# Performance work log

Hardware: AMD Instinct MI355X
Metric: run time of the kernel (lower is better)

The kernel has to match this reference:

```python
import jax, jax.numpy as jnp
import numpy as np


def _mlp(x, W1, b1, W2, b2):
    # x: (B, M, T); torch MLPLayer: transpose(1,2) -> Linear -> Linear -> LeakyReLU -> transpose back
    h = jnp.einsum('bmt,hm->bht', x, W1) + b1[None, :, None]   # (B, H, T)
    y = jnp.einsum('bht,oh->bot', h, W2) + b2[None, :, None]   # (B, M, T)
    return jax.nn.leaky_relu(y, negative_slope=0.01)


def _calc_attn(q, k, v):
    # q: (B, M, Tq), k: (B, M, Tk), v: (B, M, Tk)
    Tq = q.shape[-1]
    qk = jnp.einsum('bmq,bmk->bqk', q, k)                       # (B, Tq, Tk)
    eye = jnp.eye(Tq, dtype=qk.dtype)                           # broadcasts: (Tq,Tq) or (1,1)
    logits = jnp.exp(qk - qk * eye / jnp.sqrt(jnp.asarray(Tq, qk.dtype)))
    scores = jax.nn.softmax(logits, axis=-1)
    return jnp.einsum('bqk,bmk->bmq', scores, v)                # (B, M, Tq)


def setup_inputs() -> dict:
    key = jax.random.key(0)
    B, M, T, H = 16, 128, 2048, 512
    ks = jax.random.split(key, 14)
    s = 0.02
    inp = {
        'pattern': jax.random.normal(ks[0], (B, M, T), jnp.float32),
        'value': jax.random.normal(ks[1], (B, M, T), jnp.float32),
        'kernel_size': 33,
    }
    names = ['q', 'k', 'o']
    for i, n in enumerate(names):
        inp['W%s1' % n] = jax.random.normal(ks[2 + 4 * i], (H, M), jnp.float32) * s
        inp['b%s1' % n] = jax.random.normal(ks[3 + 4 * i], (H,), jnp.float32) * s
        inp['W%s2' % n] = jax.random.normal(ks[4 + 4 * i], (M, H), jnp.float32) * s
        inp['b%s2' % n] = jax.random.normal(ks[5 + 4 * i], (M,), jnp.float32) * s
    return inp


def reference(pattern, value, kernel_size, Wq1, bq1, Wq2, bq2, Wk1, bk1, Wk2, bk2, Wo1, bo1, Wo2, bo2):
    query = _mlp(pattern, Wq1, bq1, Wq2, bq2)
    key = _mlp(pattern, Wk1, bk1, Wk2, bk2)
    # full (internal) attention
    attn_in = _calc_attn(query, key, value)                     # (B, M, T)
    rep_in = _mlp(attn_in, Wo1, bo1, Wo2, bo2)
    # windowed (external) attention
    T = query.shape[-1]
    cu = (kernel_size - 1) // 2
    q_w = query[..., T - 1 - cu : T - cu]                       # (B, M, 1)
    k_w = key[..., kernel_size - cu - 1 : T - cu - 2]           # (B, M, T-k-1)
    v_w = value[..., kernel_size : T - 1]                       # (B, M, T-k-1)
    attn_ex = _calc_attn(q_w, k_w, v_w)                         # (B, M, 1)
    rep_ex = _mlp(attn_ex, Wo1, bo1, Wo2, bo2)
    return jnp.concatenate([rep_in, rep_ex], axis=-1)           # (B, M, T+1)
```

## Files before the change

### kernel.cpp

```cpp
#include <hip/hip_runtime.h>
#include <hip/hip_bf16.h>
#include <math.h>

#define B_    16
#define M_    128
#define T_    2048
#define H_    512
#define TOUT_ 2049

typedef unsigned short u16;
typedef unsigned int   u32;
typedef __bf16 bf16x8 __attribute__((ext_vector_type(8)));
typedef float  f32x16 __attribute__((ext_vector_type(16)));
typedef float  f32x4  __attribute__((ext_vector_type(4)));
typedef u32    u32x4  __attribute__((ext_vector_type(4)));
typedef u32    u32x2  __attribute__((ext_vector_type(2)));

#define A_OFF     0
#define C_OFF     16384
#define MEAN_OFF  16896
#define AQKBF_OFF 19200
#define AOBF_OFF  35584
#define QT_OFF    43776
#define KT_OFF    (43776 + 2097152)
#define VB_OFF    (43776 + 2 * 2097152)

static __device__ __forceinline__ u16 f2bf(float f) {
  u32 u = __float_as_uint(f);
  u = (u + 0x7FFFu + ((u >> 16) & 1u)) >> 16;
  return (u16)u;
}
static __device__ __forceinline__ u32 pk2(float lo, float hi) {
  __hip_bfloat162 h = __float22bfloat162_rn(float2{lo, hi});
  u32 r;
  __builtin_memcpy(&r, &h, 4);
  return r;
}
static __device__ __forceinline__ bf16x8 ldfrag(const u16* p) {
  return __builtin_bit_cast(bf16x8, *(const u32x4*)p);
}
static __device__ __forceinline__ float ex2(float x) {
#if __has_builtin(__builtin_amdgcn_exp2f)
  return __builtin_amdgcn_exp2f(x);
#else
  return exp2f(x);
#endif
}

__global__ __launch_bounds__(128) void fuse_weights_all(
    const float* __restrict__ W1q, const float* __restrict__ b1q,
    const float* __restrict__ W2q, const float* __restrict__ b2q,
    const float* __restrict__ W1k, const float* __restrict__ b1k,
    const float* __restrict__ W2k, const float* __restrict__ b2k,
    const float* __restrict__ W1o, const float* __restrict__ b1o,
    const float* __restrict__ W2o, const float* __restrict__ b2o,
    float* __restrict__ A, float* __restrict__ c,
    u16* __restrict__ Aqk_bf, u16* __restrict__ Ao_bf) {
  __shared__ float w2row[H_];
  int which = blockIdx.x >> 7;
  int o = blockIdx.x & 127;
  const float* W1 = which == 0 ? W1q : which == 1 ? W1k : W1o;
  const float* b1 = which == 0 ? b1q : which == 1 ? b1k : b1o;
  const float* W2 = which == 0 ? W2q : which == 1 ? W2k : W2o;
  const float* b2 = which == 0 ? b2q : which == 1 ? b2k : b2o;
  int m = threadIdx.x;
  for (int h = m; h < H_; h += 128) w2row[h] = W2[o * H_ + h];
  __syncthreads();
  float acc = 0.f;
#pragma unroll 8
  for (int h = 0; h < H_; ++h) acc = fmaf(w2row[h], W1[h * M_ + m], acc);
  u16 ab = f2bf(acc);
  if (which == 0)      Aqk_bf[o * 128 + m] = ab;
  else if (which == 1) Aqk_bf[(128 + o) * 128 + m] = ab;
  else               { Ao_bf[o * 128 + m] = ab; A[o * M_ + m] = acc; }
  if (m < 64) {
    float cc = 0.f;
    for (int h = m; h < H_; h += 64) cc = fmaf(w2row[h], b1[h], cc);
#pragma unroll
    for (int off = 32; off > 0; off >>= 1) cc += __shfl_down(cc, off, 64);
    if (m == 0) c[which * 128 + o] = cc + b2[o];
  }
}

#define XS 68

__global__ __launch_bounds__(256) void prep_kernel(
    const float* __restrict__ pattern, const u16* __restrict__ Aqk_bf,
    const float* __restrict__ cqk, u16* __restrict__ qT, u16* __restrict__ kT,
    const float* __restrict__ value, u16* __restrict__ vb,
    float* __restrict__ meanv) {
  __shared__ alignas(16) float xsf[128 * XS];
  int bx = blockIdx.x;
  int tid = threadIdx.x;

  if (bx >= 512) {
    int bm = bx - 512;
    float* red = xsf;
    const float* row = value + (size_t)bm * T_;
    int i0 = tid * 8;
    float4 a = *(const float4*)(row + i0);
    float4 bq = *(const float4*)(row + i0 + 4);
    u32x4 o = {pk2(a.x, a.y), pk2(a.z, a.w), pk2(bq.x, bq.y), pk2(bq.z, bq.w)};
    *(u32x4*)&vb[(size_t)bm * T_ + i0] = o;
    float vals[8] = {a.x, a.y, a.z, a.w, bq.x, bq.y, bq.z, bq.w};
    float s = 0.f;
#pragma unroll
    for (int j = 0; j < 8; ++j) {
      int idx = i0 + j;
      if (idx >= 33 && idx < T_ - 1) s += vals[j];
    }
    red[tid] = s;
    __syncthreads();
    for (int st = 128; st > 0; st >>= 1) {
      if (tid < st) red[tid] += red[tid + st];
      __syncthreads();
    }
    if (tid == 0) meanv[bm] = red[0] * (1.f / 2014.f);
    return;
  }

  int b = bx >> 5;
  int t0 = (bx & 31) * 64;
  int lane = tid & 63;
  int wv = tid >> 6;
  int l31 = lane & 31;
  int lh8 = (lane >> 5) * 8;

  bf16x8 afr[2][8];
#pragma unroll
  for (int i = 0; i < 2; ++i) {
    const u16* ap = Aqk_bf + ((2 * wv + i) * 32 + l31) * 128 + lh8;
#pragma unroll
    for (int s = 0; s < 8; ++s) afr[i][s] = ldfrag(ap + 16 * s);
  }

#pragma unroll
  for (int rep = 0; rep < 8; ++rep) {
    int m = rep * 16 + (tid >> 4);
    int tc = (tid & 15) * 4;
    float4 v = *(const float4*)&pattern[(size_t)(b * M_ + m) * T_ + t0 + tc];
    *(float4*)&xsf[m * XS + tc] = v;
  }
  __syncthreads();

  bf16x8 bfr[2][8];
#pragma unroll
  for (int tt = 0; tt < 2; ++tt) {
#pragma unroll
    for (int s = 0; s < 8; ++s) {
      float v0 = xsf[(s * 16 + lh8 + 0) * XS + tt * 32 + l31];
      float v1 = xsf[(s * 16 + lh8 + 1) * XS + tt * 32 + l31];
      float v2 = xsf[(s * 16 + lh8 + 2) * XS + tt * 32 + l31];
      float v3 = xsf[(s * 16 + lh8 + 3) * XS + tt * 32 + l31];
      float v4 = xsf[(s * 16 + lh8 + 4) * XS + tt * 32 + l31];
      float v5 = xsf[(s * 16 + lh8 + 5) * XS + tt * 32 + l31];
      float v6 = xsf[(s * 16 + lh8 + 6) * XS + tt * 32 + l31];
      float v7 = xsf[(s * 16 + lh8 + 7) * XS + tt * 32 + l31];
      u32x4 p = {pk2(v0, v1), pk2(v2, v3), pk2(v4, v5), pk2(v6, v7)};
      bfr[tt][s] = __builtin_bit_cast(bf16x8, p);
    }
  }
  __syncthreads();

  u16* obuf = (u16*)xsf;
#pragma unroll
  for (int tt = 0; tt < 2; ++tt) {
#pragma unroll
    for (int i = 0; i < 2; ++i) {
      f32x16 acc;
#pragma unroll
      for (int r = 0; r < 16; ++r) acc[r] = 0.f;
#pragma unroll
      for (int s = 0; s < 8; ++s)
        acc = __builtin_amdgcn_mfma_f32_32x32x16_bf16(afr[i][s], bfr[tt][s], acc, 0, 0, 0);
      int ot = 2 * wv + i;
      int t = tt * 32 + l31;
      float sc = (ot < 4) ? 1.44269504f : 1.0f;
#pragma unroll
      for (int r = 0; r < 16; ++r) {
        int orow = (r & 3) + 8 * (r >> 2) + 4 * (lane >> 5);
        float v = acc[r] + cqk[ot * 32 + orow];
        v = v > 0.f ? v : 0.01f * v;
        obuf[t * 258 + ot * 32 + orow] = f2bf(v * sc);
      }
    }
  }
  __syncthreads();

  const u32* ob32 = (const u32*)obuf;
#pragma unroll
  for (int g = 0; g < 8; ++g) {
    int G = wv * 8 + g;
    int mat = G >> 4;
    int t = (G & 15) * 4 + (lane >> 4);
    int og2 = lane & 15;
    int wbase = t * 129 + mat * 64 + og2 * 4;
    u32x4 vv = {ob32[wbase], ob32[wbase + 1], ob32[wbase + 2], ob32[wbase + 3]};
    u32* dst = (u32*)((mat ? kT : qT) + ((size_t)(b * T_ + t0 + t)) * 128) + og2 * 4;
    *(u32x4*)dst = vv;
  }
}

#define QSTR 136
#define VSTR 72
#define PSTR 72
#define PTSTR 136
#define KTILE 64
#define NKT  (T_ / KTILE)
#define CINIT 0.52876637f

__global__ __launch_bounds__(1024, 4) void attn_mfma_kernel(
    const u16* __restrict__ qT, const u16* __restrict__ kT,
    const u16* __restrict__ vB, const u16* __restrict__ Ao_bf,
    const float* __restrict__ co, const float* __restrict__ Aofp,
    const float* __restrict__ meanv, float* __restrict__ out) {
  extern __shared__ u16 smem[];
  u16* ks0 = smem;
  u16* ks1 = smem + 8704;
  u16* vs0 = smem + 17408;
  u16* vs1 = smem + 26624;
  u16* pls = smem + 35840;
  float* dls   = (float*)smem;
  u16*   ptbuf = smem + 17408;

  int b = blockIdx.y;
  int q0 = blockIdx.x * 128;
  int tid = threadIdx.x;
  int lane = tid & 63;
  int wv = tid >> 6;
  int l31 = lane & 31;
  int h = lane >> 5;
  int lh8 = h * 8;
  int qt = wv & 3;
  int ksl = wv >> 2;
  int mt = wv >> 2;

  const u16* gkb = kT + (size_t)b * T_ * 128;
  const u16* gvb = vB + (size_t)b * M_ * T_;

  bf16x8 qfrag[8];
  if (wv < 8) {
    const u16* qrow = qT + (size_t)(b * T_ + q0 + qt * 32 + l31) * 128 + lh8;
#pragma unroll
    for (int s = 0; s < 8; ++s) qfrag[s] = ldfrag(qrow + s * 16);
  }

  {
    int kr = tid >> 4, kc = (tid & 15) * 8;
    int vr = tid >> 3, vc = (tid & 7) * 8;
    *(u32x4*)&ks0[kr * QSTR + kc] = *(const u32x4*)&gkb[(size_t)kr * 128 + kc];
    *(u32x4*)&vs0[vr * VSTR + vc] = *(const u32x4*)&gvb[(size_t)vr * T_ + vc];
  }

  f32x16 pacc;
  float den = 0.f;
#pragma unroll
  for (int i = 0; i < 16; ++i) pacc[i] = 0.f;

  int t9 = tid & 511;

  for (int kt = 0; kt < NKT; ++kt) {
    u16* kcur = (kt & 1) ? ks1 : ks0;
    u16* knxt = (kt & 1) ? ks0 : ks1;
    u16* vcur = (kt & 1) ? vs1 : vs0;
    u16* vnxt = (kt & 1) ? vs0 : vs1;
    __syncthreads();

    u32x4 kr0, kr1, vr0, vr1;
    if (wv < 8) {
      f32x16 sacc;
#pragma unroll
      for (int i = 0; i < 16; ++i) sacc[i] = CINIT;
      {
        const u16* krow = &kcur[(ksl * 32 + l31) * QSTR + lh8];
#pragma unroll
        for (int s = 0; s < 8; ++s) {
          bf16x8 kf = ldfrag(krow + s * 16);
          sacc = __builtin_amdgcn_mfma_f32_32x32x16_bf16(kf, qfrag[s], sacc, 0, 0, 0);
        }
      }
      if (kt * KTILE + ksl * 32 == q0 + qt * 32) {
#pragma unroll
        for (int r = 0; r < 16; ++r) {
          int row = (r & 3) + 8 * (r >> 2) + 4 * h;
          if (row == l31) sacc[r] = fmaf(sacc[r], 0.97790291f, 0.01168420f);
        }
      }
      float w[16];
#pragma unroll
      for (int r = 0; r < 16; ++r) w[r] = ex2(ex2(sacc[r]));
      {
        float d0 = (w[0] + w[1]) + (w[2] + w[3]);
        float d1 = (w[4] + w[5]) + (w[6] + w[7]);
        float d2 = (w[8] + w[9]) + (w[10] + w[11]);
        float d3 = (w[12] + w[13]) + (w[14] + w[15]);
        den += (d0 + d1) + (d2 + d3);
      }
      u16* prow = &pls[(qt * 32 + l31) * PSTR + ksl * 32 + 4 * h];
#pragma unroll
      for (int g = 0; g < 4; ++g) {
        u32x2 wp = {pk2(w[4 * g], w[4 * g + 1]), pk2(w[4 * g + 2], w[4 * g + 3])};
        *(u32x2*)&prow[8 * g] = wp;
      }
    } else if (kt < NKT - 1) {
      int kn = (kt + 1) * KTILE;
      int ka0 = t9 >> 4, kb0 = (t9 & 15) * 8;
      int va0 = t9 >> 3, vb0 = (t9 & 7) * 8;
      kr0 = *(const u32x4*)&gkb[(size_t)(kn + ka0) * 128 + kb0];
      kr1 = *(const u32x4*)&gkb[(size_t)(kn + ka0 + 32) * 128 + kb0];
      vr0 = *(const u32x4*)&gvb[(size_t)va0 * T_ + kn + vb0];
      vr1 = *(const u32x4*)&gvb[(size_t)(va0 + 64) * T_ + kn + vb0];
    }

    __syncthreads();

    {
      const u16* vrow = &vcur[(mt * 32 + l31) * VSTR + lh8];
      const u16* prow = &pls[(qt * 32 + l31) * PSTR + lh8];
#pragma unroll
      for (int k16 = 0; k16 < 4; ++k16) {
        bf16x8 vf = ldfrag(vrow + k16 * 16);
        bf16x8 pf = ldfrag(prow + k16 * 16);
        pacc = __builtin_amdgcn_mfma_f32_32x32x16_bf16(vf, pf, pacc, 0, 0, 0);
      }
    }

    if (wv >= 8 && kt < NKT - 1) {
      int ka0 = t9 >> 4, kb0 = (t9 & 15) * 8;
      int va0 = t9 >> 3, vb0 = (t9 & 7) * 8;
      *(u32x4*)&knxt[ka0 * QSTR + kb0] = kr0;
      *(u32x4*)&knxt[(ka0 + 32) * QSTR + kb0] = kr1;
      *(u32x4*)&vnxt[va0 * VSTR + vb0] = vr0;
      *(u32x4*)&vnxt[(va0 + 64) * VSTR + vb0] = vr1;
    }
  }

  __syncthreads();
  float dq = den + __shfl_xor(den, 32, 64);
  if (wv < 8 && lane < 32) dls[ksl * 128 + qt * 32 + l31] = dq;
  __syncthreads();

  {
    float rden = 1.f / (dls[qt * 32 + l31] + dls[128 + qt * 32 + l31]);
    u16* pt = &ptbuf[(qt * 32 + l31) * PTSTR + mt * 32 + 4 * h];
#pragma unroll
    for (int g = 0; g < 4; ++g) {
      u32x2 wp = {pk2(pacc[4 * g] * rden, pacc[4 * g + 1] * rden),
                  pk2(pacc[4 * g + 2] * rden, pacc[4 * g + 3] * rden)};
      *(u32x2*)&pt[8 * g] = wp;
    }
  }
  __syncthreads();

  bf16x8 aofr[8];
  {
    const u16* ap = Ao_bf + ((wv & 3) * 32 + l31) * 128 + lh8;
#pragma unroll
    for (int s = 0; s < 8; ++s) aofr[s] = ldfrag(ap + 16 * s);
  }
  {
    int qt2 = wv >> 2;
    bf16x8 pfr[8];
    const u16* pp = &ptbuf[(qt2 * 32 + l31) * PTSTR + lh8];
#pragma unroll
    for (int s = 0; s < 8; ++s) pfr[s] = ldfrag(pp + 16 * s);
    f32x16 oacc;
#pragma unroll
    for (int r = 0; r < 16; ++r) oacc[r] = 0.f;
#pragma unroll
    for (int s = 0; s < 8; ++s)
      oacc = __builtin_amdgcn_mfma_f32_32x32x16_bf16(aofr[s], pfr[s], oacc, 0, 0, 0);
#pragma unroll
    for (int r = 0; r < 16; ++r) {
      int orow = (wv & 3) * 32 + (r & 3) + 8 * (r >> 2) + 4 * h;
      float v = oacc[r] + co[orow];
      v = v > 0.f ? v : 0.01f * v;
      out[((size_t)(b * M_ + orow)) * TOUT_ + q0 + qt2 * 32 + l31] = v;
    }
  }

  if (blockIdx.x == 0 && tid < 128) {
    float acc = co[tid];
    const float* mv = meanv + b * 128;
    for (int m = 0; m < 128; ++m) acc = fmaf(Aofp[tid * 128 + m], mv[m], acc);
    acc = acc > 0.f ? acc : 0.01f * acc;
    out[((size_t)(b * M_ + tid)) * TOUT_ + 2048] = acc;
  }
}

extern "C" void kernel_launch(void* const* d_in, const int* in_sizes, int n_in,
                              void* d_out, int out_size, void* d_ws, size_t ws_size,
                              hipStream_t stream) {
  (void)in_sizes; (void)n_in; (void)out_size; (void)ws_size;
  const float* pattern = (const float*)d_in[0];
  const float* value   = (const float*)d_in[1];
  const float* Wq1 = (const float*)d_in[3];
  const float* bq1 = (const float*)d_in[4];
  const float* Wq2 = (const float*)d_in[5];
  const float* bq2 = (const float*)d_in[6];
  const float* Wk1 = (const float*)d_in[7];
  const float* bk1 = (const float*)d_in[8];
  const float* Wk2 = (const float*)d_in[9];
  const float* bk2 = (const float*)d_in[10];
  const float* Wo1 = (const float*)d_in[11];
  const float* bo1 = (const float*)d_in[12];
  const float* Wo2 = (const float*)d_in[13];
  const float* bo2 = (const float*)d_in[14];

  float* ws     = (float*)d_ws;
  float* A      = ws + A_OFF;
  float* c      = ws + C_OFF;
  float* meanv  = ws + MEAN_OFF;
  u16*   Aqk_bf = (u16*)(ws + AQKBF_OFF);
  u16*   Ao_bf  = (u16*)(ws + AOBF_OFF);
  u16*   qT     = (u16*)(ws + QT_OFF);
  u16*   kT     = (u16*)(ws + KT_OFF);
  u16*   vB     = (u16*)(ws + VB_OFF);
  float* out    = (float*)d_out;

  fuse_weights_all<<<384, 128, 0, stream>>>(
      Wq1, bq1, Wq2, bq2, Wk1, bk1, Wk2, bk2, Wo1, bo1, Wo2, bo2,
      A, c, Aqk_bf, Ao_bf);

  prep_kernel<<<512 + B_ * M_, 256, 0, stream>>>(
      pattern, Aqk_bf, c, qT, kT, value, vB, meanv);

  size_t lds_bytes = 90112;
  attn_mfma_kernel<<<dim3(T_ / 128, B_), 1024, lds_bytes, stream>>>(
      qT, kT, vB, Ao_bf, c + 256, A, meanv, out);
}
```

Baseline: 195.3 us.

## Pipeline attention across warp groups with triple-buffered V and double-buffered P

The attention loop is restructured so producer waves (0-7) compute scores and softmax weights for tile i while consumer waves (8-15) run the P·V MFMAs for tile i-1 and prefetch K/V two tiles ahead. P gets a double buffer and V a triple buffer, which removes one barrier per iteration and overlaps exp work with the PV matmul. The cost is more LDS (about 125 KB) and all PV work sitting on half the waves, each holding two accumulators. The value-to-bf16 conversion and mean reduction move from prep_kernel into the weight-fusion kernel so they run alongside the weight fusion instead of in prep.

```diff
diff --git a/kernel.cpp b/kernel.cpp
--- a/kernel.cpp
+++ b/kernel.cpp
@@ -55,15 +55,50 @@
     const float* __restrict__ W1o, const float* __restrict__ b1o,
     const float* __restrict__ W2o, const float* __restrict__ b2o,
     float* __restrict__ A, float* __restrict__ c,
-    u16* __restrict__ Aqk_bf, u16* __restrict__ Ao_bf) {
+    u16* __restrict__ Aqk_bf, u16* __restrict__ Ao_bf,
+    const float* __restrict__ value, u16* __restrict__ vb,
+    float* __restrict__ meanv) {
   __shared__ float w2row[H_];
+  int tid = threadIdx.x;
+
+  if (blockIdx.x >= 384) {
+    int bm = blockIdx.x - 384;
+    float* red = w2row;
+    const float* row = value + (size_t)bm * T_;
+    int i0 = tid * 16;
+    float4 a0 = *(const float4*)(row + i0);
+    float4 a1 = *(const float4*)(row + i0 + 4);
+    float4 a2 = *(const float4*)(row + i0 + 8);
+    float4 a3 = *(const float4*)(row + i0 + 12);
+    u32x4 o0 = {pk2(a0.x, a0.y), pk2(a0.z, a0.w), pk2(a1.x, a1.y), pk2(a1.z, a1.w)};
+    u32x4 o1 = {pk2(a2.x, a2.y), pk2(a2.z, a2.w), pk2(a3.x, a3.y), pk2(a3.z, a3.w)};
+    *(u32x4*)&vb[(size_t)bm * T_ + i0] = o0;
+    *(u32x4*)&vb[(size_t)bm * T_ + i0 + 8] = o1;
+    float vals[16] = {a0.x, a0.y, a0.z, a0.w, a1.x, a1.y, a1.z, a1.w,
+                      a2.x, a2.y, a2.z, a2.w, a3.x, a3.y, a3.z, a3.w};
+    float s = 0.f;
+#pragma unroll
+    for (int j = 0; j < 16; ++j) {
+      int idx = i0 + j;
+      if (idx >= 33 && idx < T_ - 1) s += vals[j];
+    }
+    red[tid] = s;
+    __syncthreads();
+    for (int st = 64; st > 0; st >>= 1) {
+      if (tid < st) red[tid] += red[tid + st];
+      __syncthreads();
+    }
+    if (tid == 0) meanv[bm] = red[0] * (1.f / 2014.f);
+    return;
+  }
+
   int which = blockIdx.x >> 7;
   int o = blockIdx.x & 127;
   const float* W1 = which == 0 ? W1q : which == 1 ? W1k : W1o;
   const float* b1 = which == 0 ? b1q : which == 1 ? b1k : b1o;
   const float* W2 = which == 0 ? W2q : which == 1 ? W2k : W2o;
   const float* b2 = which == 0 ? b2q : which == 1 ? b2k : b2o;
-  int m = threadIdx.x;
+  int m = tid;
   for (int h = m; h < H_; h += 128) w2row[h] = W2[o * H_ + h];
   __syncthreads();
   float acc = 0.f;
@@ -86,38 +121,10 @@
 
 __global__ __launch_bounds__(256) void prep_kernel(
     const float* __restrict__ pattern, const u16* __restrict__ Aqk_bf,
-    const float* __restrict__ cqk, u16* __restrict__ qT, u16* __restrict__ kT,
-    const float* __restrict__ value, u16* __restrict__ vb,
-    float* __restrict__ meanv) {
+    const float* __restrict__ cqk, u16* __restrict__ qT, u16* __restrict__ kT) {
   __shared__ alignas(16) float xsf[128 * XS];
   int bx = blockIdx.x;
   int tid = threadIdx.x;
-
-  if (bx >= 512) {
-    int bm = bx - 512;
-    float* red = xsf;
-    const float* row = value + (size_t)bm * T_;
-    int i0 = tid * 8;
-    float4 a = *(const float4*)(row + i0);
-    float4 bq = *(const float4*)(row + i0 + 4);
-    u32x4 o = {pk2(a.x, a.y), pk2(a.z, a.w), pk2(bq.x, bq.y), pk2(bq.z, bq.w)};
-    *(u32x4*)&vb[(size_t)bm * T_ + i0] = o;
-    float vals[8] = {a.x, a.y, a.z, a.w, bq.x, bq.y, bq.z, bq.w};
-    float s = 0.f;
-#pragma unroll
-    for (int j = 0; j < 8; ++j) {
-      int idx = i0 + j;
-      if (idx >= 33 && idx < T_ - 1) s += vals[j];
-    }
-    red[tid] = s;
-    __syncthreads();
-    for (int st = 128; st > 0; st >>= 1) {
-      if (tid < st) red[tid] += red[tid + st];
-      __syncthreads();
-    }
-    if (tid == 0) meanv[bm] = red[0] * (1.f / 2014.f);
-    return;
-  }
 
   int b = bx >> 5;
   int t0 = (bx & 31) * 64;
@@ -215,13 +222,15 @@
     const float* __restrict__ co, const float* __restrict__ Aofp,
     const float* __restrict__ meanv, float* __restrict__ out) {
   extern __shared__ u16 smem[];
-  u16* ks0 = smem;
-  u16* ks1 = smem + 8704;
-  u16* vs0 = smem + 17408;
-  u16* vs1 = smem + 26624;
-  u16* pls = smem + 35840;
-  float* dls   = (float*)smem;
-  u16*   ptbuf = smem + 17408;
+  u16* kb0 = smem;
+  u16* kb1 = smem + 8704;
+  u16* vbf0 = smem + 17408;
+  u16* vbf1 = smem + 26624;
+  u16* vbf2 = smem + 35840;
+  u16* pb0 = smem + 45056;
+  u16* pb1 = smem + 54272;
+  float* dls = (float*)(smem + 63488);
+  u16* ptbuf = smem;
 
   int b = blockIdx.y;
   int q0 = blockIdx.x * 128;
@@ -231,15 +240,18 @@
   int l31 = lane & 31;
   int h = lane >> 5;
   int lh8 = h * 8;
+  bool prod = wv < 8;
   int qt = wv & 3;
-  int ksl = wv >> 2;
-  int mt = wv >> 2;
+  int ksl = (wv >> 2) & 1;
+  int cw = wv & 7;
+  int mt = cw & 3;
+  int qh = cw >> 2;
 
   const u16* gkb = kT + (size_t)b * T_ * 128;
   const u16* gvb = vB + (size_t)b * M_ * T_;
 
   bf16x8 qfrag[8];
-  if (wv < 8) {
+  if (prod) {
     const u16* qrow = qT + (size_t)(b * T_ + q0 + qt * 32 + l31) * 128 + lh8;
 #pragma unroll
     for (int s = 0; s < 8; ++s) qfrag[s] = ldfrag(qrow + s * 16);
@@ -248,106 +260,125 @@
   {
     int kr = tid >> 4, kc = (tid & 15) * 8;
     int vr = tid >> 3, vc = (tid & 7) * 8;
-    *(u32x4*)&ks0[kr * QSTR + kc] = *(const u32x4*)&gkb[(size_t)kr * 128 + kc];
-    *(u32x4*)&vs0[vr * VSTR + vc] = *(const u32x4*)&gvb[(size_t)vr * T_ + vc];
-  }
-
-  f32x16 pacc;
+    *(u32x4*)&kb0[kr * QSTR + kc] = *(const u32x4*)&gkb[(size_t)kr * 128 + kc];
+    *(u32x4*)&vbf0[vr * VSTR + vc] = *(const u32x4*)&gvb[(size_t)vr * T_ + vc];
+  }
+
+  int ct = tid & 511;
+  int kr0 = ct >> 4, kc0 = (ct & 15) * 8;
+  int vr0 = ct >> 3, vc0 = (ct & 7) * 8;
+  u32x4 kreg0, kreg1, vreg0, vreg1;
+  if (!prod) {
+    kreg0 = *(const u32x4*)&gkb[(size_t)(KTILE + kr0) * 128 + kc0];
+    kreg1 = *(const u32x4*)&gkb[(size_t)(KTILE + kr0 + 32) * 128 + kc0];
+    vreg0 = *(const u32x4*)&gvb[(size_t)vr0 * T_ + KTILE + vc0];
+    vreg1 = *(const u32x4*)&gvb[(size_t)(vr0 + 64) * T_ + KTILE + vc0];
+  }
+
+  f32x16 pacc0, pacc1;
   float den = 0.f;
 #pragma unroll
-  for (int i = 0; i < 16; ++i) pacc[i] = 0.f;
-
-  int t9 = tid & 511;
-
-  for (int kt = 0; kt < NKT; ++kt) {
-    u16* kcur = (kt & 1) ? ks1 : ks0;
-    u16* knxt = (kt & 1) ? ks0 : ks1;
-    u16* vcur = (kt & 1) ? vs1 : vs0;
-    u16* vnxt = (kt & 1) ? vs0 : vs1;
+  for (int i = 0; i < 16; ++i) { pacc0[i] = 0.f; pacc1[i] = 0.f; }
+
+  u16* vprev = vbf2;
+  u16* vcur  = vbf0;
+  u16* vnxt  = vbf1;
+
+  __syncthreads();
+
+  for (int i = 0; i <= NKT; ++i) {
+    if (prod) {
+      if (i < NKT) {
+        u16* kcur = (i & 1) ? kb1 : kb0;
+        f32x16 sacc;
+#pragma unroll
+        for (int r = 0; r < 16; ++r) sacc[r] = CINIT;
+        {
+          const u16* krow = &kcur[(ksl * 32 + l31) * QSTR + lh8];
+#pragma unroll
+          for (int s = 0; s < 8; ++s) {
+            bf16x8 kf = ldfrag(krow + s * 16);
+            sacc = __builtin_amdgcn_mfma_f32_32x32x16_bf16(kf, qfrag[s], sacc, 0, 0, 0);
+          }
+        }
+        if (i * KTILE + ksl * 32 == q0 + qt * 32) {
+#pragma unroll
+          for (int r = 0; r < 16; ++r) {
+            int row = (r & 3) + 8 * (r >> 2) + 4 * h;
+            if (row == l31) sacc[r] = fmaf(sacc[r], 0.97790291f, 0.01168420f);
+          }
+        }
+        float w[16];
+#pragma unroll
+        for (int r = 0; r < 16; ++r) w[r] = ex2(ex2(sacc[r]));
+        {
+          float d0 = (w[0] + w[1]) + (w[2] + w[3]);
+          float d1 = (w[4] + w[5]) + (w[6] + w[7]);
+          float d2 = (w[8] + w[9]) + (w[10] + w[11]);
+          float d3 = (w[12] + w[13]) + (w[14] + w[15]);
+          den += (d0 + d1) + (d2 + d3);
+        }
+        u16* pw = (i & 1) ? pb1 : pb0;
+        u16* prow = &pw[(qt * 32 + l31) * PSTR + ksl * 32 + 4 * h];
+#pragma unroll
+        for (int g = 0; g < 4; ++g) {
+          u32x2 wp = {pk2(w[4 * g], w[4 * g + 1]), pk2(w[4 * g + 2], w[4 * g + 3])};
+          *(u32x2*)&prow[8 * g] = wp;
+        }
+      }
+    } else {
+      if (i + 1 < NKT) {
+        u16* kw = ((i + 1) & 1) ? kb1 : kb0;
+        *(u32x4*)&kw[kr0 * QSTR + kc0] = kreg0;
+        *(u32x4*)&kw[(kr0 + 32) * QSTR + kc0] = kreg1;
+        *(u32x4*)&vnxt[vr0 * VSTR + vc0] = vreg0;
+        *(u32x4*)&vnxt[(vr0 + 64) * VSTR + vc0] = vreg1;
+      }
+      if (i >= 1) {
+        const u16* pr = ((i - 1) & 1) ? pb1 : pb0;
+        const u16* vrow = &vprev[(mt * 32 + l31) * VSTR + lh8];
+        const u16* prow0 = &pr[((qh * 2) * 32 + l31) * PSTR + lh8];
+        const u16* prow1 = &pr[((qh * 2 + 1) * 32 + l31) * PSTR + lh8];
+#pragma unroll
+        for (int k16 = 0; k16 < 4; ++k16) {
+          bf16x8 vf = ldfrag(vrow + k16 * 16);
+          bf16x8 pf0 = ldfrag(prow0 + k16 * 16);
+          bf16x8 pf1 = ldfrag(prow1 + k16 * 16);
+          pacc0 = __builtin_amdgcn_mfma_f32_32x32x16_bf16(vf, pf0, pacc0, 0, 0, 0);
+          pacc1 = __builtin_amdgcn_mfma_f32_32x32x16_bf16(vf, pf1, pacc1, 0, 0, 0);
+        }
+      }
+      if (i + 2 < NKT) {
+        int kn2 = (i + 2) * KTILE;
+        kreg0 = *(const u32x4*)&gkb[(size_t)(kn2 + kr0) * 128 + kc0];
+        kreg1 = *(const u32x4*)&gkb[(size_t)(kn2 + kr0 + 32) * 128 + kc0];
+        vreg0 = *(const u32x4*)&gvb[(size_t)vr0 * T_ + kn2 + vc0];
+        vreg1 = *(const u32x4*)&gvb[(size_t)(vr0 + 64) * T_ + kn2 + vc0];
+      }
+    }
+    u16* tmp = vprev; vprev = vcur; vcur = vnxt; vnxt = tmp;
     __syncthreads();
-
-    u32x4 kr0, kr1, vr0, vr1;
-    if (wv < 8) {
-      f32x16 sacc;
-#pragma unroll
-      for (int i = 0; i < 16; ++i) sacc[i] = CINIT;
-      {
-        const u16* krow = &kcur[(ksl * 32 + l31) * QSTR + lh8];
-#pragma unroll
-        for (int s = 0; s < 8; ++s) {
-          bf16x8 kf = ldfrag(krow + s * 16);
-          sacc = __builtin_amdgcn_mfma_f32_32x32x16_bf16(kf, qfrag[s], sacc, 0, 0, 0);
-        }
-      }
-      if (kt * KTILE + ksl * 32 == q0 + qt * 32) {
-#pragma unroll
-        for (int r = 0; r < 16; ++r) {
-          int row = (r & 3) + 8 * (r >> 2) + 4 * h;
-          if (row == l31) sacc[r] = fmaf(sacc[r], 0.97790291f, 0.01168420f);
-        }
-      }
-      float w[16];
-#pragma unroll
-      for (int r = 0; r < 16; ++r) w[r] = ex2(ex2(sacc[r]));
-      {
-        float d0 = (w[0] + w[1]) + (w[2] + w[3]);
-        float d1 = (w[4] + w[5]) + (w[6] + w[7]);
-        float d2 = (w[8] + w[9]) + (w[10] + w[11]);
-        float d3 = (w[12] + w[13]) + (w[14] + w[15]);
-        den += (d0 + d1) + (d2 + d3);
-      }
-      u16* prow = &pls[(qt * 32 + l31) * PSTR + ksl * 32 + 4 * h];
+  }
+
+  if (prod) {
+    float dq = den + __shfl_xor(den, 32, 64);
+    if (lane < 32) dls[ksl * 128 + qt * 32 + l31] = dq;
+  }
+  __syncthreads();
+
+  if (!prod) {
+#pragma unroll
+    for (int j = 0; j < 2; ++j) {
+      int qt2 = qh * 2 + j;
+      float rden = 1.f / (dls[qt2 * 32 + l31] + dls[128 + qt2 * 32 + l31]);
+      const f32x16& pa = j ? pacc1 : pacc0;
+      u16* pt = &ptbuf[(qt2 * 32 + l31) * PTSTR + mt * 32 + 4 * h];
 #pragma unroll
       for (int g = 0; g < 4; ++g) {
-        u32x2 wp = {pk2(w[4 * g], w[4 * g + 1]), pk2(w[4 * g + 2], w[4 * g + 3])};
-        *(u32x2*)&prow[8 * g] = wp;
-      }
-    } else if (kt < NKT - 1) {
-      int kn = (kt + 1) * KTILE;
-      int ka0 = t9 >> 4, kb0 = (t9 & 15) * 8;
-      int va0 = t9 >> 3, vb0 = (t9 & 7) * 8;
-      kr0 = *(const u32x4*)&gkb[(size_t)(kn + ka0) * 128 + kb0];
-      kr1 = *(const u32x4*)&gkb[(size_t)(kn + ka0 + 32) * 128 + kb0];
-      vr0 = *(const u32x4*)&gvb[(size_t)va0 * T_ + kn + vb0];
-      vr1 = *(const u32x4*)&gvb[(size_t)(va0 + 64) * T_ + kn + vb0];
-    }
-
-    __syncthreads();
-
-    {
-      const u16* vrow = &vcur[(mt * 32 + l31) * VSTR + lh8];
-      const u16* prow = &pls[(qt * 32 + l31) * PSTR + lh8];
-#pragma unroll
-      for (int k16 = 0; k16 < 4; ++k16) {
-        bf16x8 vf = ldfrag(vrow + k16 * 16);
-        bf16x8 pf = ldfrag(prow + k16 * 16);
-        pacc = __builtin_amdgcn_mfma_f32_32x32x16_bf16(vf, pf, pacc, 0, 0, 0);
-      }
-    }
-
-    if (wv >= 8 && kt < NKT - 1) {
-      int ka0 = t9 >> 4, kb0 = (t9 & 15) * 8;
-      int va0 = t9 >> 3, vb0 = (t9 & 7) * 8;
-      *(u32x4*)&knxt[ka0 * QSTR + kb0] = kr0;
-      *(u32x4*)&knxt[(ka0 + 32) * QSTR + kb0] = kr1;
-      *(u32x4*)&vnxt[va0 * VSTR + vb0] = vr0;
-      *(u32x4*)&vnxt[(va0 + 64) * VSTR + vb0] = vr1;
-    }
-  }
-
-  __syncthreads();
-  float dq = den + __shfl_xor(den, 32, 64);
-  if (wv < 8 && lane < 32) dls[ksl * 128 + qt * 32 + l31] = dq;
-  __syncthreads();
-
-  {
-    float rden = 1.f / (dls[qt * 32 + l31] + dls[128 + qt * 32 + l31]);
-    u16* pt = &ptbuf[(qt * 32 + l31) * PTSTR + mt * 32 + 4 * h];
-#pragma unroll
-    for (int g = 0; g < 4; ++g) {
-      u32x2 wp = {pk2(pacc[4 * g] * rden, pacc[4 * g + 1] * rden),
-                  pk2(pacc[4 * g + 2] * rden, pacc[4 * g + 3] * rden)};
-      *(u32x2*)&pt[8 * g] = wp;
+        u32x2 wp = {pk2(pa[4 * g] * rden, pa[4 * g + 1] * rden),
+                    pk2(pa[4 * g + 2] * rden, pa[4 * g + 3] * rden)};
+        *(u32x2*)&pt[8 * g] = wp;
+      }
     }
   }
   __syncthreads();
@@ -418,14 +449,13 @@
   u16*   vB     = (u16*)(ws + VB_OFF);
   float* out    = (float*)d_out;
 
-  fuse_weights_all<<<384, 128, 0, stream>>>(
+  fuse_weights_all<<<384 + B_ * M_, 128, 0, stream>>>(
       Wq1, bq1, Wq2, bq2, Wk1, bk1, Wk2, bk2, Wo1, bo1, Wo2, bo2,
-      A, c, Aqk_bf, Ao_bf);
-
-  prep_kernel<<<512 + B_ * M_, 256, 0, stream>>>(
-      pattern, Aqk_bf, c, qT, kT, value, vB, meanv);
-
-  size_t lds_bytes = 90112;
+      A, c, Aqk_bf, Ao_bf, value, vB, meanv);
+
+  prep_kernel<<<512, 256, 0, stream>>>(pattern, Aqk_bf, c, qT, kT);
+
+  size_t lds_bytes = 128000;
   attn_mfma_kernel<<<dim3(T_ / 128, B_), 1024, lds_bytes, stream>>>(
       qT, kT, vB, Ao_bf, c + 256, A, meanv, out);
 }
```

Result: faster. 189.2 us (-3.1%).
